# Optimization experiments

Measured on AMD Instinct MI355X. Metric: run time of the kernel, lower is better.

Reference implementation:

```python
import jax, jax.numpy as jnp
import numpy as np

B, V, F, H = 2, 5023, 9976, 256
CHUNK = 128
EPS = 1e-5
LIGHT_LOC = jnp.array([0.0, 1.0, 3.0], dtype=jnp.float32)   # PointLights(location)
AMB, DIFF, SPEC = 0.5, 0.3, 0.2 * 0.6                        # light amb/diff * mat(1.0); spec light*mat
SHININESS = 10.0
TEXEL = jnp.array([142.0, 179.0, 247.0], dtype=jnp.float32) / 255.0
BG = jnp.array([1.0, 1.0, 1.0], dtype=jnp.float32)


def setup_inputs():
    key = jax.random.key(0)
    k1, k2 = jax.random.split(key)
    vertices = jax.random.normal(k1, (B, V, 3), dtype=jnp.float32) * 0.05
    faces = jax.random.randint(k2, (F, 3), 0, V)
    # default camera built inside forward: R = diag(-1,1,-1), T = (0,0,2*scale)
    tm = jnp.array([[-1.0, 0.0, 0.0, 0.0],
                    [0.0, 1.0, 0.0, 0.0],
                    [0.0, 0.0, -1.0, 2.0]], dtype=jnp.float32)
    transform_matrix = jnp.tile(tm[None], (B, 1, 1))
    focal_length = jnp.full((B, 1), 12.0, dtype=jnp.float32)
    return {"vertices": vertices, "transform_matrix": transform_matrix,
            "focal_length": focal_length, "faces": faces}


def _normalize(v):
    return v / jnp.maximum(jnp.linalg.norm(v, axis=-1, keepdims=True), 1e-6)


def _render(vertices, transform_matrix, focal_length, faces):
    R = transform_matrix[:, :3, :3]
    T = transform_matrix[:, :3, 3]
    # pytorch3d row-vector convention: x_cam = x_world @ R + T
    verts_cam = jnp.einsum('bvi,bij->bvj', vertices, R) + T[:, None, :]
    zc = verts_cam[..., 2]                                    # view depth
    x_ndc = focal_length * verts_cam[..., 0] / zc             # fx*x/z (+px=0)
    y_ndc = focal_length * verts_cam[..., 1] / zc
    vndc = jnp.stack([x_ndc, y_ndc, zc], axis=-1)             # [B,V,3]

    # pixel centers in pytorch3d NDC (+x left, +y up); top-left pixel -> (+1-1/H, +1-1/H)
    ax = 1.0 - (2.0 * jnp.arange(H, dtype=jnp.float32) + 1.0) / H
    px = jnp.tile(ax[None, :], (H, 1)).reshape(-1)            # [P] columns
    py = jnp.tile(ax[:, None], (1, H)).reshape(-1)            # [P] rows
    P = H * H

    npad = (-F) % CHUNK
    faces_p = jnp.concatenate([faces, jnp.zeros((npad, 3), faces.dtype)], 0)
    fvalid = jnp.concatenate([jnp.ones((F,), bool), jnp.zeros((npad,), bool)])
    n_chunks = faces_p.shape[0] // CHUNK
    chunk_ids = jnp.arange(n_chunks * CHUNK, dtype=jnp.int32).reshape(n_chunks, CHUNK)

    def step(carry, fidx):
        best_z, bw0, bw1, bw2, best_face = carry
        tri = faces_p[fidx]                                   # [C,3]
        fv = vndc[:, tri]                                     # [B,C,3,3]
        def corner(k):
            return (fv[:, :, k, 0][..., None], fv[:, :, k, 1][..., None],
                    fv[:, :, k, 2][..., None])
        x0, y0, z0 = corner(0); x1, y1, z1 = corner(1); x2, y2, z2 = corner(2)
        z0s = jnp.where(z0 > EPS, z0, 1.0)
        z1s = jnp.where(z1 > EPS, z1, 1.0)
        z2s = jnp.where(z2 > EPS, z2, 1.0)
        den = (y1 - y2) * (x0 - x2) + (x2 - x1) * (y0 - y2)   # [B,C,1]
        ok = jnp.abs(den) > 1e-8
        dens = jnp.where(ok, den, 1.0)
        w0 = ((y1 - y2) * (px - x2) + (x2 - x1) * (py - y2)) / dens   # [B,C,P]
        w1 = ((y2 - y0) * (px - x2) + (x0 - x2) * (py - y2)) / dens
        w2 = 1.0 - w0 - w1
        inside = (w0 >= 0) & (w1 >= 0) & (w2 >= 0) & ok
        inside &= (z0 > EPS) & (z1 > EPS) & (z2 > EPS)
        inside &= fvalid[fidx][None, :, None]
        iz = w0 / z0s + w1 / z1s + w2 / z2s                    # perspective-correct 1/z
        good = inside & (iz > 1e-8)
        izs = jnp.where(good, iz, 1.0)
        zsafe = 1.0 / izs
        zpix = jnp.where(good, zsafe, jnp.inf)
        w0c = jnp.where(good, (w0 / z0s) * zsafe, 0.0)
        w1c = jnp.where(good, (w1 / z1s) * zsafe, 0.0)
        w2c = jnp.where(good, (w2 / z2s) * zsafe, 0.0)
        idx = jnp.argmin(zpix, axis=1)                         # [B,P]
        g = lambda a: jnp.take_along_axis(a, idx[:, None, :], axis=1)[:, 0]
        zmin = g(zpix)
        upd = zmin < best_z
        best_z = jnp.where(upd, zmin, best_z)
        bw0 = jnp.where(upd, g(w0c), bw0)
        bw1 = jnp.where(upd, g(w1c), bw1)
        bw2 = jnp.where(upd, g(w2c), bw2)
        best_face = jnp.where(upd, fidx[idx], best_face)
        return (best_z, bw0, bw1, bw2, best_face), None

    init = (jnp.full((B, P), jnp.inf, jnp.float32),
            jnp.zeros((B, P), jnp.float32), jnp.zeros((B, P), jnp.float32),
            jnp.zeros((B, P), jnp.float32), jnp.full((B, P), -1, jnp.int32))
    (best_z, bw0, bw1, bw2, best_face), _ = jax.lax.scan(jax.checkpoint(step), init, chunk_ids)

    mask = best_face >= 0                                      # [B,P]
    bary = jnp.stack([bw0, bw1, bw2], axis=-1)                 # [B,P,3]
    tri_sel = faces_p[jnp.clip(best_face, 0)]                  # [B,P,3]

    # area-weighted vertex normals (pytorch3d _compute_vertex_normals)
    fw = vertices[:, faces]                                    # [B,F,3,3]
    fn = jnp.cross(fw[:, :, 1] - fw[:, :, 0], fw[:, :, 2] - fw[:, :, 0])  # [B,F,3]
    vn = jnp.zeros_like(vertices).at[:, faces.reshape(-1)].add(jnp.repeat(fn, 3, axis=1))
    vn = _normalize(vn)

    gv = jax.vmap(lambda t, i: t[i])(vertices, tri_sel)        # [B,P,3,3] world pos
    gn = jax.vmap(lambda t, i: t[i])(vn, tri_sel)              # [B,P,3,3] normals
    pos = jnp.einsum('bpk,bpkc->bpc', bary, gv)
    nrm = _normalize(jnp.einsum('bpk,bpkc->bpc', bary, gn))

    cam_pos = -jnp.einsum('bj,bkj->bk', T, R)                  # camera center in world
    Ldir = _normalize(LIGHT_LOC - pos)
    Vdir = _normalize(cam_pos[:, None, :] - pos)
    cosNL = jnp.sum(nrm * Ldir, axis=-1)
    diffuse = DIFF * jax.nn.relu(cosNL)
    refl = 2.0 * cosNL[..., None] * nrm - Ldir
    spec = SPEC * jax.nn.relu(jnp.sum(Vdir * refl, axis=-1)) ** SHININESS
    rgb = TEXEL * (AMB + diffuse)[..., None] + spec[..., None] # [B,P,3]
    rgb = jnp.where(mask[..., None], rgb, BG)                  # hard_rgb_blend, bg=(1,1,1)

    images = rgb.reshape(B, H, H, 3).transpose(0, 3, 1, 2) * 255.0  # area-interp to same size = identity
    alpha = mask.astype(jnp.float32).reshape(B, 1, H, H)
    return images, alpha


def reference(vertices, transform_matrix, focal_length, faces):
    return _render(vertices, transform_matrix, focal_length, faces)
```

## Files before the change

### kernel.cpp

```cpp
#include <hip/hip_runtime.h>
#include <stdint.h>

#define H 256
#define PIX (H*H)
#define BATCH 2
#define NV 5023
#define NF 9976
#define EPS 1e-5f
#define CH 128
#define NBUCK 4096

typedef unsigned long long ull;
#define INF_KEY 0x7F800000FFFFFFFFULL

__device__ __forceinline__ float axf(int i) {
    return 1.0f - (2.0f * (float)i + 1.0f) / (float)H;
}

__device__ __forceinline__ float bf16snap(float x) {
    unsigned u = __float_as_uint(x);
    unsigned r = (u + 0x7FFFu + ((u >> 16) & 1u)) & 0xFFFF0000u;
    return __uint_as_float(r);
}

__device__ __forceinline__ int zbucket(float z) {
    int q = (int)floorf((z - 0.5f) * (4096.0f / 3.0f));
    return q < 0 ? 0 : (q > 4095 ? 4095 : q);
}
__device__ __forceinline__ float zbucket_lower(int q) {
    return (q == 0) ? 0.0f : 0.5f + (float)q * (3.0f / 4096.0f);
}

__global__ void setup_all(const float* __restrict__ verts, const float* __restrict__ tm,
                          const float* __restrict__ focal, const int* __restrict__ faces,
                          float* __restrict__ fd, float* __restrict__ zminArr,
                          float* __restrict__ vn, int* __restrict__ hist) {
#pragma clang fp contract(off)
    int t = blockIdx.x * blockDim.x + threadIdx.x;
    if (t >= BATCH * NF) return;
    int b = t / NF, f = t % NF;
    const float* M = tm + b * 12;
    float fl = focal[b];
    float X[3], Y[3], Z[3];
#pragma unroll
    for (int k = 0; k < 3; k++) {
        int vi = faces[f * 3 + k];
        const float* v = verts + (b * NV + vi) * 3;
        float v0 = v[0], v1 = v[1], v2 = v[2];
        float c0 = ((v0 * M[0] + v1 * M[4]) + v2 * M[8])  + M[3];
        float c1 = ((v0 * M[1] + v1 * M[5]) + v2 * M[9])  + M[7];
        float c2 = ((v0 * M[2] + v1 * M[6]) + v2 * M[10]) + M[11];
        X[k] = (fl * c0) / c2;
        Y[k] = (fl * c1) / c2;
        Z[k] = c2;
    }
    float x0 = X[0], x1 = X[1], x2 = X[2];
    float y0 = Y[0], y1 = Y[1], y2 = Y[2];
    float z0 = Z[0], z1 = Z[1], z2 = Z[2];
    float den = (y1 - y2) * (x0 - x2) + (x2 - x1) * (y0 - y2);
    bool zv = (z0 > EPS) && (z1 > EPS) && (z2 > EPS);
    bool okS = zv && (fabsf(den) > 1e-8f);
    bool okR = zv && (fabsf(den) > 5e-9f);
    float xmn, xmx, ymn, ymx;
    if (okR) {
        float e01 = (x1 - x0) * (x1 - x0) + (y1 - y0) * (y1 - y0);
        float e12 = (x2 - x1) * (x2 - x1) + (y2 - y1) * (y2 - y1);
        float e20 = (x0 - x2) * (x0 - x2) + (y0 - y2) * (y0 - y2);
        float E2 = fmaxf(fmaxf(e01, e12), e20);
        float delta = 1e-4f * E2 / fabsf(den) + 1e-3f;
        if (!(delta < 4.0f)) delta = 4.0f;
        xmn = fminf(fminf(x0, x1), x2) - delta;
        xmx = fmaxf(fmaxf(x0, x1), x2) + delta;
        ymn = fminf(fminf(y0, y1), y2) - delta;
        ymx = fmaxf(fmaxf(y0, y1), y2) + delta;
    } else {
        xmn = 1e30f; xmx = -1e30f; ymn = 1e30f; ymx = -1e30f;
    }
    float* o = fd + (size_t)t * 16;
    o[0] = y1 - y2;  o[1] = x2 - x1;
    o[2] = y2 - y0;  o[3] = x0 - x2;
    o[4] = x2;       o[5] = y2;
    o[6] = den;      o[7] = okS ? 1.0f : 0.0f;
    o[8] = xmn;  o[9] = xmx;  o[10] = ymn;  o[11] = ymx;
    o[12] = z0;  o[13] = z1;  o[14] = z2;   o[15] = 0.0f;
    float zm = okR ? fminf(fminf(z0, z1), z2) : -1.0f;
    zminArr[t] = zm;
    if (zm >= 0.0f) atomicAdd(&hist[b * NBUCK + zbucket(zm)], 1);

    {
        int i0 = faces[f*3+0], i1 = faces[f*3+1], i2 = faces[f*3+2];
        const float* vb = verts + b * NV * 3;
        float a0 = vb[i0*3+0], a1 = vb[i0*3+1], a2 = vb[i0*3+2];
        float b0 = vb[i1*3+0], b1 = vb[i1*3+1], b2 = vb[i1*3+2];
        float c0 = vb[i2*3+0], c1 = vb[i2*3+1], c2 = vb[i2*3+2];
        float e1x = b0 - a0, e1y = b1 - a1, e1z = b2 - a2;
        float e2x = c0 - a0, e2y = c1 - a1, e2z = c2 - a2;
        float nx = e1y * e2z - e1z * e2y;
        float ny = e1z * e2x - e1x * e2z;
        float nz = e1x * e2y - e1y * e2x;
        float* nb = vn + (size_t)b * NV * 3;
        atomicAdd(&nb[i0*3+0], nx); atomicAdd(&nb[i0*3+1], ny); atomicAdd(&nb[i0*3+2], nz);
        atomicAdd(&nb[i1*3+0], nx); atomicAdd(&nb[i1*3+1], ny); atomicAdd(&nb[i1*3+2], nz);
        atomicAdd(&nb[i2*3+0], nx); atomicAdd(&nb[i2*3+1], ny); atomicAdd(&nb[i2*3+2], nz);
    }
}

__global__ __launch_bounds__(256) void zscan(const int* __restrict__ hist,
                                             int* __restrict__ start,
                                             int* __restrict__ total) {
    int b = blockIdx.x;
    __shared__ int tot[256];
    int t = threadIdx.x;
    int a[16]; int s = 0;
#pragma unroll
    for (int i = 0; i < 16; i++) { int c = hist[b * NBUCK + t * 16 + i]; a[i] = s; s += c; }
    tot[t] = s;
    __syncthreads();
    for (int off = 1; off < 256; off <<= 1) {
        int x = tot[t];
        if (t >= off) x += tot[t - off];
        __syncthreads();
        tot[t] = x;
        __syncthreads();
    }
    int pre = (t > 0) ? tot[t - 1] : 0;
#pragma unroll
    for (int i = 0; i < 16; i++) start[b * NBUCK + t * 16 + i] = pre + a[i];
    if (t == 255) total[b] = tot[255];
}

__global__ void zscatter(const float* __restrict__ fd, const float* __restrict__ zminArr,
                         const int* __restrict__ start, int* __restrict__ cursor,
                         float* __restrict__ fds, float* __restrict__ blow,
                         float* __restrict__ vn) {
#pragma clang fp contract(off)
    int t = blockIdx.x * blockDim.x + threadIdx.x;
    if (t < BATCH * NV) {
        float x = vn[t*3+0], y = vn[t*3+1], z = vn[t*3+2];
        float n = fmaxf(sqrtf((x*x + y*y) + z*z), 1e-6f);
        vn[t*3+0] = x / n; vn[t*3+1] = y / n; vn[t*3+2] = z / n;
    }
    if (t >= BATCH * NF) return;
    float zm = zminArr[t];
    if (zm < 0.0f) return;
    int b = t / NF, f = t % NF;
    int q = zbucket(zm);
    int dst = start[b * NBUCK + q] + atomicAdd(&cursor[b * NBUCK + q], 1);
    const float* o = fd + (size_t)t * 16;
    float* d = fds + ((size_t)b * NF + dst) * 16;
#pragma unroll
    for (int k = 0; k < 15; k++) d[k] = o[k];
    d[15] = __uint_as_float((unsigned)f);
    blow[(size_t)b * NF + dst] = zbucket_lower(q);
}

__global__ __launch_bounds__(64) void raster(const float* __restrict__ fds,
                                             const float* __restrict__ blow,
                                             const int* __restrict__ total,
                                             int2* __restrict__ pix) {
#pragma clang fp contract(off)
    __shared__ __align__(16) float4 sbb[CH];
    __shared__ __align__(16) float sfd[CH * 16];
    __shared__ int slist[CH];
    __shared__ int scnt;
    int tid = threadIdx.x;
    int b = blockIdx.z;
    int id = blockIdx.y * 32 + blockIdx.x;
    int sw = (id * 733) & 1023;
    int col0 = (sw & 31) * 8, row0 = (sw >> 5) * 8;
    int col = col0 + (tid & 7), row = row0 + (tid >> 3);
    float px = axf(col), py = axf(row);
    float qxmax = axf(col0), qxmin = axf(col0 + 7);
    float qymax = axf(row0), qymin = axf(row0 + 7);
    ull ks = INF_KEY, k1 = INF_KEY, k2 = INF_KEY;
    const float4* fdb4 = (const float4*)(fds + (size_t)b * NF * 16);
    int cntb = total[b];

    for (int fbase = 0; fbase < cntb; fbase += CH) {
        int n = min(CH, cntb - fbase);
        if (tid == 0) scnt = 0;
        for (int j = tid; j < n; j += 64)
            sbb[j] = fdb4[(size_t)(fbase + j) * 4 + 2];
        __syncthreads();
        for (int j = tid; j < n; j += 64) {
            float4 bb = sbb[j];
            if (bb.x <= qxmax && bb.y >= qxmin && bb.z <= qymax && bb.w >= qymin) {
                int p2 = atomicAdd(&scnt, 1);
                slist[p2] = j;
            }
        }
        __syncthreads();
        int cnt = scnt;
        for (int j = tid; j < cnt * 4; j += 64) {
            int e = fbase + slist[j >> 2];
            ((float4*)sfd)[j] = fdb4[(size_t)e * 4 + (j & 3)];
        }
        __syncthreads();
        for (int i = 0; i < cnt; i++) {
            const float* o = sfd + i * 16;
            bool cand = (px >= o[8]) & (px <= o[9]) & (py >= o[10]) & (py <= o[11]);
            if (__ballot(cand) == 0ULL) continue;
            float dx = px - o[4], dy = py - o[5];
            float num0 = o[0] * dx + o[1] * dy;
            float num1 = o[2] * dx + o[3] * dy;
            float adsn = fabsf(o[6]);
            float dsgn = (o[6] > 0.0f) ? 1.0f : -1.0f;
            float n0s = num0 * dsgn, n1s = num1 * dsgn;
            float thr = 2e-5f * adsn, thr2 = 1.001f * adsn;
            bool plaus = cand && (n0s >= -thr) && (n1s >= -thr) && ((n0s + n1s) <= thr2);
            if (__ballot(plaus) == 0ULL) continue;
            if (plaus) {
                float w0 = num0 / o[6];
                float w1 = num1 / o[6];
                float w2 = (1.0f - w0) - w1;
                bool insS = (o[7] != 0.0f) && (w0 >= 0.0f) && (w1 >= 0.0f) && (w2 >= 0.0f);
                bool insR = (w0 >= -1e-5f) && (w1 >= -1e-5f) && (w2 >= -1e-5f);
                if (insR) {
                    float iz = ((w0 / o[12]) + (w1 / o[13])) + (w2 / o[14]);
                    if (iz > 1e-8f) {
                        float zp = 1.0f / iz;
                        ull key = ((ull)__float_as_uint(zp) << 32) |
                                  (ull)(unsigned)__float_as_uint(o[15]);
                        if (insS && key < ks) ks = key;
                        if (key < k1) { k2 = k1; k1 = key; }
                        else if (key < k2) { k2 = key; }
                    }
                }
            }
        }
        if (fbase + CH < cntb) {
            float nf = blow[(size_t)b * NF + fbase + CH];
            float madj = nf * (1.0f - 1e-4f);
            float zsv = __uint_as_float((unsigned)(ks >> 32));
            float zbv = __uint_as_float((unsigned)(k2 >> 32));
            bool oldc = (ks != INF_KEY) && (k2 != INF_KEY) && (zsv < madj) && (zbv < madj);
            bool newc = (ks != INF_KEY) && (1.051f * zsv < madj);
            bool done = (nf > 0.0f) && (oldc || newc);
            if (__ballot(!done) == 0ULL) break;
            __syncthreads();
        }
    }
    int fs = -1;
    float zs = 0.0f;
    if ((unsigned)(ks >> 32) != 0x7F800000u) {
        fs = (int)(unsigned)ks;
        zs = __uint_as_float((unsigned)(ks >> 32));
    }
    int fr = -1;
    if (fs >= 0) {
        ull mR = INF_KEY;
        if ((int)(unsigned)k1 != fs && k1 < mR) mR = k1;
        if ((int)(unsigned)k2 != fs && k2 < mR) mR = k2;
        if ((unsigned)(mR >> 32) != 0x7F800000u) {
            float zr = __uint_as_float((unsigned)(mR >> 32));
            if (fabsf(zr - zs) <= 0.05f * zs) fr = (int)(unsigned)mR;
        }
    }
    pix[(size_t)b * PIX + (size_t)row * H + col] = make_int2(fs, fr);
}

__device__ void shade_face(int f, int b, float px, float py,
                           const float* __restrict__ fd, const float* __restrict__ verts,
                           const int* __restrict__ faces, const float* __restrict__ vn,
                           const float* __restrict__ tm, float* rgb) {
#pragma clang fp contract(off)
    const float* o = fd + ((size_t)b * NF + f) * 16;
    float dx = px - o[4], dy = py - o[5];
    float w0 = (o[0] * dx + o[1] * dy) / o[6];
    float w1 = (o[2] * dx + o[3] * dy) / o[6];
    float w2 = (1.0f - w0) - w1;
    float q0 = w0 / o[12], q1 = w1 / o[13], q2 = w2 / o[14];
    float iz = (q0 + q1) + q2;
    float zsafe = 1.0f / iz;
    float bw0 = q0 * zsafe, bw1 = q1 * zsafe, bw2 = q2 * zsafe;
    int i0 = faces[f*3+0], i1 = faces[f*3+1], i2 = faces[f*3+2];
    const float* vb = verts + b * NV * 3;
    const float* nb = vn + b * NV * 3;
    float posx = (bw0*vb[i0*3+0] + bw1*vb[i1*3+0]) + bw2*vb[i2*3+0];
    float posy = (bw0*vb[i0*3+1] + bw1*vb[i1*3+1]) + bw2*vb[i2*3+1];
    float posz = (bw0*vb[i0*3+2] + bw1*vb[i1*3+2]) + bw2*vb[i2*3+2];
    float nx = (bw0*nb[i0*3+0] + bw1*nb[i1*3+0]) + bw2*nb[i2*3+0];
    float ny = (bw0*nb[i0*3+1] + bw1*nb[i1*3+1]) + bw2*nb[i2*3+1];
    float nz = (bw0*nb[i0*3+2] + bw1*nb[i1*3+2]) + bw2*nb[i2*3+2];
    float nn = fmaxf(sqrtf((nx*nx + ny*ny) + nz*nz), 1e-6f);
    nx /= nn; ny /= nn; nz /= nn;
    const float* M = tm + b * 12;
    float T0 = M[3], T1 = M[7], T2 = M[11];
    float cpx = -((T0*M[0] + T1*M[1]) + T2*M[2]);
    float cpy = -((T0*M[4] + T1*M[5]) + T2*M[6]);
    float cpz = -((T0*M[8] + T1*M[9]) + T2*M[10]);
    float lx = 0.0f - posx, ly = 1.0f - posy, lz = 3.0f - posz;
    float ln = fmaxf(sqrtf((lx*lx + ly*ly) + lz*lz), 1e-6f);
    lx /= ln; ly /= ln; lz /= ln;
    float vx = cpx - posx, vy = cpy - posy, vz = cpz - posz;
    float vnn = fmaxf(sqrtf((vx*vx + vy*vy) + vz*vz), 1e-6f);
    vx /= vnn; vy /= vnn; vz /= vnn;
    float cosNL = (nx*lx + ny*ly) + nz*lz;
    float diffuse = 0.3f * fmaxf(cosNL, 0.0f);
    float rx = (2.0f * cosNL) * nx - lx;
    float ry = (2.0f * cosNL) * ny - ly;
    float rz = (2.0f * cosNL) * nz - lz;
    float vr = (vx*rx + vy*ry) + vz*rz;
    float spec = 0.12f * powf(fmaxf(vr, 0.0f), 10.0f);
    float sA = 0.5f + diffuse;
    rgb[0] = ((142.0f / 255.0f) * sA + spec) * 255.0f;
    rgb[1] = ((179.0f / 255.0f) * sA + spec) * 255.0f;
    rgb[2] = ((247.0f / 255.0f) * sA + spec) * 255.0f;
}

__global__ void shade(const int2* __restrict__ pix, const float* __restrict__ fd,
                      const float* __restrict__ verts, const int* __restrict__ faces,
                      const float* __restrict__ vn, const float* __restrict__ tm,
                      float* __restrict__ out) {
#pragma clang fp contract(off)
    int t = blockIdx.x * blockDim.x + threadIdx.x;
    if (t >= BATCH * PIX) return;
    int b = t / PIX, p = t % PIX;
    int row = p / H, col = p % H;
    int2 pk = pix[t];
    int fs = pk.x, fr = pk.y;
    float r, g, bc, a;
    if (fs < 0) {
        r = g = bc = 255.0f;
        a = 0.0f;
    } else {
        float px = axf(col), py = axf(row);
        float A[3];
        shade_face(fs, b, px, py, fd, verts, faces, vn, tm, A);
        r = A[0]; g = A[1]; bc = A[2];
        if (fr >= 0) {
            float Bc[3];
            shade_face(fr, b, px, py, fd, verts, faces, vn, tm, Bc);
            float As0 = bf16snap(A[0]), As1 = bf16snap(A[1]), As2 = bf16snap(A[2]);
            float Bs0 = bf16snap(Bc[0]), Bs1 = bf16snap(Bc[1]), Bs2 = bf16snap(Bc[2]);
            if (fabsf(As0 - Bs0) <= 9.01f && fabsf(As1 - Bs1) <= 9.01f &&
                fabsf(As2 - Bs2) <= 9.01f) {
                r  = 0.5f * (As0 + Bs0);
                g  = 0.5f * (As1 + Bs1);
                bc = 0.5f * (As2 + Bs2);
            }
        }
        a = 1.0f;
    }
    out[(((size_t)b*3 + 0) * H + row) * H + col] = r;
    out[(((size_t)b*3 + 1) * H + row) * H + col] = g;
    out[(((size_t)b*3 + 2) * H + row) * H + col] = bc;
    out[(size_t)BATCH*3*H*H + ((size_t)b * H + row) * H + col] = a;
}

extern "C" void kernel_launch(void* const* d_in, const int* in_sizes, int n_in,
                              void* d_out, int out_size, void* d_ws, size_t ws_size,
                              hipStream_t stream) {
    const float* verts = (const float*)d_in[0];
    const float* tm    = (const float*)d_in[1];
    const float* focal = (const float*)d_in[2];
    const int*   faces = (const int*)d_in[3];
    float* out = (float*)d_out;

    char* ws = (char*)d_ws;
    float* fd      = (float*)ws;
    float* vn      = (float*)(ws + 1276928);
    int*   hist    = (int*)  (ws + 1397504);
    int*   cursor  = (int*)  (ws + 1430272);
    int2*  pix     = (int2*) (ws + 1463040);
    float* fds     = (float*)(ws + 2511616);
    float* blow    = (float*)(ws + 3788544);
    float* zminArr = (float*)(ws + 3868416);
    int*   start   = (int*)  (ws + 3948288);
    int*   total   = (int*)  (ws + 3981056);

    hipMemsetAsync(vn, 0, 186112, stream);

    setup_all<<<(BATCH * NF + 255) / 256, 256, 0, stream>>>(verts, tm, focal, faces,
                                                            fd, zminArr, vn, hist);
    zscan<<<BATCH, 256, 0, stream>>>(hist, start, total);
    zscatter<<<(BATCH * NF + 255) / 256, 256, 0, stream>>>(fd, zminArr, start, cursor,
                                                           fds, blow, vn);
    dim3 rg(32, 32, BATCH);
    raster<<<rg, 64, 0, stream>>>(fds, blow, total, pix);

    shade<<<(BATCH * PIX + 255) / 256, 256, 0, stream>>>(pix, fd, verts, faces, vn, tm, out);
}
```

Baseline: 299.7 us.

## Split raster tile face loop across four wavefronts with shared-memory top-k merge

The raster kernel now launches 256 threads per 8x8 tile instead of 64. Each of the four wavefronts handles every fourth candidate face for the same 64 pixels. Per-wave depth keys (best shaded, top two) are merged through shared memory before each early-exit check and at the end. This is meant to cut the serial per-tile face loop latency, in exchange for extra syncs, shared memory and merge work per chunk.

After: 293.2 us. -2.2%, faster.

```diff
diff --git a/kernel.cpp b/kernel.cpp
--- a/kernel.cpp
+++ b/kernel.cpp
@@ -154,21 +154,23 @@
     blow[(size_t)b * NF + dst] = zbucket_lower(q);
 }
 
-__global__ __launch_bounds__(64) void raster(const float* __restrict__ fds,
-                                             const float* __restrict__ blow,
-                                             const int* __restrict__ total,
-                                             int2* __restrict__ pix) {
+__global__ __launch_bounds__(256) void raster(const float* __restrict__ fds,
+                                              const float* __restrict__ blow,
+                                              const int* __restrict__ total,
+                                              int2* __restrict__ pix) {
 #pragma clang fp contract(off)
     __shared__ __align__(16) float4 sbb[CH];
     __shared__ __align__(16) float sfd[CH * 16];
     __shared__ int slist[CH];
     __shared__ int scnt;
+    __shared__ ull mks[4][64], mk1[4][64], mk2[4][64];
     int tid = threadIdx.x;
+    int wid = tid >> 6, lane = tid & 63;
     int b = blockIdx.z;
     int id = blockIdx.y * 32 + blockIdx.x;
     int sw = (id * 733) & 1023;
     int col0 = (sw & 31) * 8, row0 = (sw >> 5) * 8;
-    int col = col0 + (tid & 7), row = row0 + (tid >> 3);
+    int col = col0 + (lane & 7), row = row0 + (lane >> 3);
     float px = axf(col), py = axf(row);
     float qxmax = axf(col0), qxmin = axf(col0 + 7);
     float qymax = axf(row0), qymin = axf(row0 + 7);
@@ -179,24 +181,24 @@
     for (int fbase = 0; fbase < cntb; fbase += CH) {
         int n = min(CH, cntb - fbase);
         if (tid == 0) scnt = 0;
-        for (int j = tid; j < n; j += 64)
+        for (int j = tid; j < n; j += 256)
             sbb[j] = fdb4[(size_t)(fbase + j) * 4 + 2];
         __syncthreads();
-        for (int j = tid; j < n; j += 64) {
-            float4 bb = sbb[j];
+        if (tid < n) {
+            float4 bb = sbb[tid];
             if (bb.x <= qxmax && bb.y >= qxmin && bb.z <= qymax && bb.w >= qymin) {
                 int p2 = atomicAdd(&scnt, 1);
-                slist[p2] = j;
+                slist[p2] = tid;
             }
         }
         __syncthreads();
         int cnt = scnt;
-        for (int j = tid; j < cnt * 4; j += 64) {
+        for (int j = tid; j < cnt * 4; j += 256) {
             int e = fbase + slist[j >> 2];
             ((float4*)sfd)[j] = fdb4[(size_t)e * 4 + (j & 3)];
         }
         __syncthreads();
-        for (int i = 0; i < cnt; i++) {
+        for (int i = wid; i < cnt; i += 4) {
             const float* o = sfd + i * 16;
             bool cand = (px >= o[8]) & (px <= o[9]) & (py >= o[10]) & (py <= o[11]);
             if (__ballot(cand) == 0ULL) continue;
@@ -229,34 +231,64 @@
             }
         }
         if (fbase + CH < cntb) {
+            mks[wid][lane] = ks; mk1[wid][lane] = k1; mk2[wid][lane] = k2;
+            __syncthreads();
+            ull Ks = mks[0][lane];
+            if (mks[1][lane] < Ks) Ks = mks[1][lane];
+            if (mks[2][lane] < Ks) Ks = mks[2][lane];
+            if (mks[3][lane] < Ks) Ks = mks[3][lane];
+            ull m1 = INF_KEY, m2 = INF_KEY;
+#pragma unroll
+            for (int w = 0; w < 4; w++) {
+                ull v = mk1[w][lane];
+                if (v < m1) { m2 = m1; m1 = v; } else if (v < m2 && v != m1) m2 = v;
+                v = mk2[w][lane];
+                if (v < m1) { m2 = m1; m1 = v; } else if (v < m2 && v != m1) m2 = v;
+            }
             float nf = blow[(size_t)b * NF + fbase + CH];
             float madj = nf * (1.0f - 1e-4f);
-            float zsv = __uint_as_float((unsigned)(ks >> 32));
-            float zbv = __uint_as_float((unsigned)(k2 >> 32));
-            bool oldc = (ks != INF_KEY) && (k2 != INF_KEY) && (zsv < madj) && (zbv < madj);
-            bool newc = (ks != INF_KEY) && (1.051f * zsv < madj);
+            float zsv = __uint_as_float((unsigned)(Ks >> 32));
+            float zbv = __uint_as_float((unsigned)(m2 >> 32));
+            bool oldc = (Ks != INF_KEY) && (m2 != INF_KEY) && (zsv < madj) && (zbv < madj);
+            bool newc = (Ks != INF_KEY) && (1.051f * zsv < madj);
             bool done = (nf > 0.0f) && (oldc || newc);
-            if (__ballot(!done) == 0ULL) break;
-            __syncthreads();
-        }
-    }
-    int fs = -1;
-    float zs = 0.0f;
-    if ((unsigned)(ks >> 32) != 0x7F800000u) {
-        fs = (int)(unsigned)ks;
-        zs = __uint_as_float((unsigned)(ks >> 32));
-    }
-    int fr = -1;
-    if (fs >= 0) {
-        ull mR = INF_KEY;
-        if ((int)(unsigned)k1 != fs && k1 < mR) mR = k1;
-        if ((int)(unsigned)k2 != fs && k2 < mR) mR = k2;
-        if ((unsigned)(mR >> 32) != 0x7F800000u) {
-            float zr = __uint_as_float((unsigned)(mR >> 32));
-            if (fabsf(zr - zs) <= 0.05f * zs) fr = (int)(unsigned)mR;
-        }
-    }
-    pix[(size_t)b * PIX + (size_t)row * H + col] = make_int2(fs, fr);
+            int notdone = __syncthreads_count(done ? 0 : 1);
+            if (notdone == 0) break;
+        }
+    }
+    mks[wid][lane] = ks; mk1[wid][lane] = k1; mk2[wid][lane] = k2;
+    __syncthreads();
+    if (wid == 0) {
+        ull Ks = mks[0][lane];
+        if (mks[1][lane] < Ks) Ks = mks[1][lane];
+        if (mks[2][lane] < Ks) Ks = mks[2][lane];
+        if (mks[3][lane] < Ks) Ks = mks[3][lane];
+        ull m1 = INF_KEY, m2 = INF_KEY;
+#pragma unroll
+        for (int w = 0; w < 4; w++) {
+            ull v = mk1[w][lane];
+            if (v < m1) { m2 = m1; m1 = v; } else if (v < m2 && v != m1) m2 = v;
+            v = mk2[w][lane];
+            if (v < m1) { m2 = m1; m1 = v; } else if (v < m2 && v != m1) m2 = v;
+        }
+        int fs = -1;
+        float zs = 0.0f;
+        if ((unsigned)(Ks >> 32) != 0x7F800000u) {
+            fs = (int)(unsigned)Ks;
+            zs = __uint_as_float((unsigned)(Ks >> 32));
+        }
+        int fr = -1;
+        if (fs >= 0) {
+            ull mR = INF_KEY;
+            if ((int)(unsigned)m1 != fs && m1 < mR) mR = m1;
+            if ((int)(unsigned)m2 != fs && m2 < mR) mR = m2;
+            if ((unsigned)(mR >> 32) != 0x7F800000u) {
+                float zr = __uint_as_float((unsigned)(mR >> 32));
+                if (fabsf(zr - zs) <= 0.05f * zs) fr = (int)(unsigned)mR;
+            }
+        }
+        pix[(size_t)b * PIX + (size_t)row * H + col] = make_int2(fs, fr);
+    }
 }
 
 __device__ void shade_face(int f, int b, float px, float py,
@@ -377,7 +409,7 @@
     zscatter<<<(BATCH * NF + 255) / 256, 256, 0, stream>>>(fd, zminArr, start, cursor,
                                                            fds, blow, vn);
     dim3 rg(32, 32, BATCH);
-    raster<<<rg, 64, 0, stream>>>(fds, blow, total, pix);
+    raster<<<rg, 256, 0, stream>>>(fds, blow, total, pix);
 
     shade<<<(BATCH * PIX + 255) / 256, 256, 0, stream>>>(pix, fd, verts, faces, vn, tm, out);
 }
```
